# Kernel tuning notes

Measured on AMD Instinct MI355X. Metric: run time of the kernel, lower is better.

## Reference

```python
import jax, jax.numpy as jnp
import numpy as np


def setup_inputs() -> dict:
    key = jax.random.key(0)
    ks = jax.random.split(key, 6)
    B, F, E, H, U = 64, 4096, 256, 512, 512
    scale = 0.02
    return {
        "features": jax.random.normal(ks[0], (B, F, E), dtype=jnp.float32),
        "hidden": jax.random.normal(ks[1], (B, H), dtype=jnp.float32),
        "W1_w": jax.random.normal(ks[2], (E, U), dtype=jnp.float32) * scale,
        "W1_b": jnp.zeros((U,), dtype=jnp.float32),
        "W2_w": jax.random.normal(ks[3], (H, U), dtype=jnp.float32) * scale,
        "W2_b": jnp.zeros((U,), dtype=jnp.float32),
        "V_w": jax.random.normal(ks[4], (U, 1), dtype=jnp.float32) * scale,
        "V_b": jnp.zeros((1,), dtype=jnp.float32),
    }


def reference(features, hidden, W1_w, W1_b, W2_w, W2_b, V_w, V_b):
    # features: (B, F, E); hidden: (B, H)
    proj_f = jnp.einsum("bfe,eu->bfu", features, W1_w) + W1_b          # (B, F, U)
    proj_h = (hidden @ W2_w + W2_b)[:, None, :]                        # (B, 1, U)
    attention_hidden = jnp.tanh(proj_f + proj_h)                       # (B, F, U)
    scores = jnp.einsum("bfu,uo->bfo", attention_hidden, V_w) + V_b    # (B, F, 1)
    attention_weights = jax.nn.softmax(scores, axis=1)                 # (B, F, 1)
    context_vector = jnp.sum(attention_weights * features, axis=1)     # (B, E)
    return (context_vector, attention_weights)
```

## Files before the change

### kernel.cpp

```cpp
#include <hip/hip_runtime.h>
#include <cmath>

constexpr int Bdim = 64;
constexpr int Fdim = 4096;
constexpr int Edim = 256;
constexpr int Hdim = 512;
constexpr int Udim = 512;

typedef __attribute__((ext_vector_type(8))) short short8;
typedef __attribute__((ext_vector_type(4))) float f32x4;

__device__ __forceinline__ unsigned short f2bf(float f) {
    unsigned int u = __float_as_uint(f);
    u += 0x7FFFu + ((u >> 16) & 1u);
    return (unsigned short)(u >> 16);
}
__device__ __forceinline__ unsigned int pack2(float lo, float hi) {
    return (unsigned int)f2bf(lo) | ((unsigned int)f2bf(hi) << 16);
}
__device__ __forceinline__ float tanh_fast(float x) {
    float e = __expf(2.0f * x);
    return 1.0f - 2.0f * __builtin_amdgcn_rcpf(e + 1.0f);
}
__device__ __forceinline__ void gload_lds16(const void* g, void* l) {
    __builtin_amdgcn_global_load_lds(
        (const __attribute__((address_space(1))) unsigned int*)g,
        (__attribute__((address_space(3))) unsigned int*)l, 16, 0, 0);
}

__global__ __launch_bounds__(256) void prep_kernel(
    const float* __restrict__ hidden, const float* __restrict__ W2,
    const float* __restrict__ W1b, const float* __restrict__ W2b,
    float* __restrict__ cb,
    const float* __restrict__ W1, unsigned short* __restrict__ Th,
    float* __restrict__ ctx, const int do_t)
{
    const int bid = blockIdx.x;
    const int tid = threadIdx.x;

    if (bid < 128) {
        const int b = bid >> 1;
        const int u = (bid & 1) * 256 + tid;
        const float* hb = hidden + (size_t)b * Hdim;
        float acc = 0.f;
        #pragma unroll 8
        for (int h = 0; h < Hdim; ++h)
            acc = fmaf(hb[h], W2[(size_t)h * Udim + u], acc);
        cb[(size_t)b * Udim + u] = acc + W1b[u] + W2b[u];
    } else if (bid < 160) {
        if (!do_t) return;
        __shared__ unsigned short sT[64][72];
        const int k  = bid - 128;
        const int e0 = (k & 3) * 64, u0 = (k >> 2) * 64;
        const int ue = tid & 63, er = tid >> 6;
        #pragma unroll
        for (int it = 0; it < 16; ++it) {
            const int e = er + it * 4;
            sT[ue][e] = f2bf(W1[(size_t)(e0 + e) * Udim + u0 + ue]);
        }
        __syncthreads();
        const int ur = tid >> 2, cq = tid & 3;
        const int u = u0 + ur, s = u & 7;
        const int cA = (e0 >> 3) + cq * 2;
        uint4 a  = *(const uint4*)&sT[ur][cq * 16];
        uint4 b2 = *(const uint4*)&sT[ur][cq * 16 + 8];
        unsigned short* dst = Th + (size_t)u * Edim;
        *(uint4*)(dst + ((cA ^ s) << 3))       = a;
        *(uint4*)(dst + (((cA + 1) ^ s) << 3)) = b2;
    } else {
        const int idx = (bid - 160) * 256 + tid;
        ((float4*)ctx)[idx] = make_float4(0.f, 0.f, 0.f, 0.f);
    }
}

__global__ __launch_bounds__(256, 4) void score_mfma4_kernel(
    const float* __restrict__ feat,
    const unsigned short* __restrict__ W1Ts,
    const float* __restrict__ Vw, const float* __restrict__ Vb,
    const float* __restrict__ cb, float* __restrict__ scr)
{
    __shared__ unsigned short lds[16896];

    const int b    = blockIdx.y;
    const int f0   = blockIdx.x * 64;
    const int tid  = threadIdx.x;
    const int lane = tid & 63;
    const int w    = tid >> 6;
    const int ln15 = lane & 15;
    const int kq   = lane >> 4;
    const int swz  = ln15 & 7;

    short8 af[8];
    {
        unsigned short* sAw = lds + w * 4224;
        const float* gA = feat + ((size_t)(b * Fdim + f0 + w * 16)) * Edim;
        #pragma unroll
        for (int r = 0; r < 16; ++r) {
            float4 v = *(const float4*)(gA + (size_t)r * Edim + lane * 4);
            uint2 p; p.x = pack2(v.x, v.y); p.y = pack2(v.z, v.w);
            *(uint2*)&sAw[r * 264 + lane * 4] = p;
        }
        #pragma unroll
        for (int k8 = 0; k8 < 8; ++k8)
            af[k8] = *(const short8*)&sAw[ln15 * 264 + k8 * 32 + kq * 8];
    }
    __syncthreads();

    float sacc[4] = {};
    const float* cbB = cb + (size_t)b * Udim;

    {
        const char* gB = (const char*)W1Ts;
        #pragma unroll
        for (int t = 0; t < 4; ++t) {
            const int chunk = w * 4 + t;
            gload_lds16(gB + (size_t)chunk * 1024 + lane * 16,
                        (char*)lds + chunk * 1024);
        }
    }
    __syncthreads();

    for (int p = 0; p < 16; ++p) {
        if (p < 15) {
            const char* gB = (const char*)(W1Ts + (size_t)(p + 1) * 32 * Edim);
            char* lb = (char*)lds + ((p + 1) & 1) * 16384;
            #pragma unroll
            for (int t = 0; t < 4; ++t) {
                const int chunk = w * 4 + t;
                gload_lds16(gB + (size_t)chunk * 1024 + lane * 16,
                            lb + chunk * 1024);
            }
        }

        const unsigned short* bw = lds + (p & 1) * 8192;
        const int ub = p * 32;
        const float cu0 = cbB[ub + ln15],     cu1 = cbB[ub + 16 + ln15];
        const float vv0 = Vw[ub + ln15],      vv1 = Vw[ub + 16 + ln15];
        f32x4 acc0 = {}, acc1 = {};
        #pragma unroll
        for (int k8 = 0; k8 < 8; ++k8) {
            const int co = ((k8 * 4 + kq) ^ swz) * 8;
            short8 b0 = *(const short8*)&bw[ln15 * 256 + co];
            short8 b1 = *(const short8*)&bw[(16 + ln15) * 256 + co];
            acc0 = __builtin_amdgcn_mfma_f32_16x16x32_bf16(af[k8], b0, acc0, 0, 0, 0);
            acc1 = __builtin_amdgcn_mfma_f32_16x16x32_bf16(af[k8], b1, acc1, 0, 0, 0);
        }
        #pragma unroll
        for (int r = 0; r < 4; ++r)
            sacc[r] += tanh_fast(acc0[r] + cu0) * vv0
                     + tanh_fast(acc1[r] + cu1) * vv1;

        if (p < 15) __syncthreads();
    }

    const float vb = Vb[0];
    #pragma unroll
    for (int r = 0; r < 4; ++r) {
        float s = sacc[r];
        s += __shfl_xor(s, 1);
        s += __shfl_xor(s, 2);
        s += __shfl_xor(s, 4);
        s += __shfl_xor(s, 8);
        if (ln15 == 0)
            scr[(size_t)b * Fdim + f0 + w * 16 + kq * 4 + r] = s + vb;
    }
}

__global__ __launch_bounds__(256) void ctxnorm_kernel(
    const float* __restrict__ feat, const float* __restrict__ scr,
    float* __restrict__ wts, float* __restrict__ ctx)
{
    __shared__ float  red[8];
    __shared__ float  wl[256];
    __shared__ float4 sred[256];

    const int b   = blockIdx.y;
    const int fc  = blockIdx.x;
    const int f0  = fc * 256;
    const int tid = threadIdx.x;
    const float* row = scr + (size_t)b * Fdim;

    float v[16];
    float m = -INFINITY;
    #pragma unroll
    for (int i = 0; i < 16; ++i) {
        v[i] = row[tid + 256 * i];
        m = fmaxf(m, v[i]);
    }
    #pragma unroll
    for (int off = 1; off < 64; off <<= 1)
        m = fmaxf(m, __shfl_xor(m, off));
    if ((tid & 63) == 0) red[tid >> 6] = m;
    __syncthreads();
    m = fmaxf(fmaxf(red[0], red[1]), fmaxf(red[2], red[3]));

    float s = 0.f;
    #pragma unroll
    for (int i = 0; i < 16; ++i)
        s += expf(v[i] - m);
    #pragma unroll
    for (int off = 1; off < 64; off <<= 1)
        s += __shfl_xor(s, off);
    if ((tid & 63) == 0) red[4 + (tid >> 6)] = s;
    __syncthreads();
    const float inv = 1.0f / (red[4] + red[5] + red[6] + red[7]);

    const float wgt = expf(v[fc] - m) * inv;
    wts[(size_t)b * Fdim + f0 + tid] = wgt;
    wl[tid] = wgt;
    __syncthreads();

    const int e4 = tid & 63;
    const int fg = tid >> 6;
    const float4* fp = (const float4*)(feat + ((size_t)b * Fdim + f0) * Edim);

    float4 a = make_float4(0.f, 0.f, 0.f, 0.f);
    #pragma unroll 8
    for (int i = 0; i < 64; ++i) {
        const int f = i * 4 + fg;
        const float4 fv = fp[(size_t)f * 64 + e4];
        const float wv = wl[f];
        a.x = fmaf(wv, fv.x, a.x);
        a.y = fmaf(wv, fv.y, a.y);
        a.z = fmaf(wv, fv.z, a.z);
        a.w = fmaf(wv, fv.w, a.w);
    }
    sred[tid] = a;
    __syncthreads();

    if (fg == 0) {
        const float4 r0 = sred[e4];
        const float4 r1 = sred[64 + e4];
        const float4 r2 = sred[128 + e4];
        const float4 r3 = sred[192 + e4];
        float* cp = ctx + (size_t)b * Edim + e4 * 4;
        atomicAdd(cp + 0, r0.x + r1.x + r2.x + r3.x);
        atomicAdd(cp + 1, r0.y + r1.y + r2.y + r3.y);
        atomicAdd(cp + 2, r0.z + r1.z + r2.z + r3.z);
        atomicAdd(cp + 3, r0.w + r1.w + r2.w + r3.w);
    }
}

constexpr int TFt = 64;
constexpr int TUt = 64;
constexpr int LDR = Edim + 4;

__global__ __launch_bounds__(256) void score_kernel(
    const float* __restrict__ feat, const float* __restrict__ W1,
    const float* __restrict__ Vw, const float* __restrict__ Vb,
    const float* __restrict__ cb, float* __restrict__ scores)
{
    __shared__ float sA[TFt * LDR];
    __shared__ float sW[TUt * LDR];

    const int b   = blockIdx.y;
    const int f0  = blockIdx.x * TFt;
    const int tid = threadIdx.x;
    const int tf  = tid >> 4;
    const int tu  = tid & 15;

    {
        const float4* gA = (const float4*)(feat + ((size_t)b * Fdim + f0) * Edim);
        #pragma unroll
        for (int it = 0; it < 16; ++it) {
            const int i = tid + it * 256;
            const int f = i >> 6;
            const int qq = i & 63;
            const float4 v = gA[i];
            *(float4*)&sA[f * LDR + 4 * qq] = v;
        }
    }

    float sacc[4] = {0.f, 0.f, 0.f, 0.f};
    const float* cbb = cb + (size_t)b * Udim;

    for (int uc = 0; uc < Udim; uc += TUt) {
        __syncthreads();
        #pragma unroll
        for (int it = 0; it < 16; ++it) {
            const int i = tid + it * 256;
            const int e = i >> 4;
            const int qq = i & 15;
            const float4 v = *(const float4*)(W1 + (size_t)e * Udim + uc + 4 * qq);
            sW[(4 * qq + 0) * LDR + e] = v.x;
            sW[(4 * qq + 1) * LDR + e] = v.y;
            sW[(4 * qq + 2) * LDR + e] = v.z;
            sW[(4 * qq + 3) * LDR + e] = v.w;
        }
        __syncthreads();

        float acc[4][4] = {};
        #pragma unroll 4
        for (int e = 0; e < Edim; e += 4) {
            float4 a0 = *(const float4*)&sA[(tf +  0) * LDR + e];
            float4 a1 = *(const float4*)&sA[(tf + 16) * LDR + e];
            float4 a2 = *(const float4*)&sA[(tf + 32) * LDR + e];
            float4 a3 = *(const float4*)&sA[(tf + 48) * LDR + e];
            float4 w0 = *(const float4*)&sW[(tu +  0) * LDR + e];
            float4 w1 = *(const float4*)&sW[(tu + 16) * LDR + e];
            float4 w2 = *(const float4*)&sW[(tu + 32) * LDR + e];
            float4 w3 = *(const float4*)&sW[(tu + 48) * LDR + e];
            #define FMA4(i, j, A, W)                         \
                acc[i][j] = fmaf(A.x, W.x, acc[i][j]);       \
                acc[i][j] = fmaf(A.y, W.y, acc[i][j]);       \
                acc[i][j] = fmaf(A.z, W.z, acc[i][j]);       \
                acc[i][j] = fmaf(A.w, W.w, acc[i][j]);
            FMA4(0,0,a0,w0) FMA4(0,1,a0,w1) FMA4(0,2,a0,w2) FMA4(0,3,a0,w3)
            FMA4(1,0,a1,w0) FMA4(1,1,a1,w1) FMA4(1,2,a1,w2) FMA4(1,3,a1,w3)
            FMA4(2,0,a2,w0) FMA4(2,1,a2,w1) FMA4(2,2,a2,w2) FMA4(2,3,a2,w3)
            FMA4(3,0,a3,w0) FMA4(3,1,a3,w1) FMA4(3,2,a3,w2) FMA4(3,3,a3,w3)
            #undef FMA4
        }

        #pragma unroll
        for (int j = 0; j < 4; ++j) {
            const int u = uc + tu + 16 * j;
            const float vw = Vw[u];
            const float cuv = cbb[u];
            #pragma unroll
            for (int i = 0; i < 4; ++i)
                sacc[i] = fmaf(tanhf(acc[i][j] + cuv), vw, sacc[i]);
        }
    }

    const float vb = Vb[0];
    #pragma unroll
    for (int i = 0; i < 4; ++i) {
        float s = sacc[i];
        s += __shfl_xor(s, 1);
        s += __shfl_xor(s, 2);
        s += __shfl_xor(s, 4);
        s += __shfl_xor(s, 8);
        if (tu == 0)
            scores[(size_t)b * Fdim + f0 + tf + 16 * i] = s + vb;
    }
}

__global__ __launch_bounds__(256) void softmax_kernel(float* __restrict__ sc)
{
    __shared__ float red[256];
    const int b = blockIdx.x;
    const int tid = threadIdx.x;
    float* row = sc + (size_t)b * Fdim;

    float v[16];
    float m = -INFINITY;
    #pragma unroll
    for (int i = 0; i < 16; ++i) {
        v[i] = row[tid + 256 * i];
        m = fmaxf(m, v[i]);
    }
    red[tid] = m;
    __syncthreads();
    for (int s = 128; s > 0; s >>= 1) {
        if (tid < s) red[tid] = fmaxf(red[tid], red[tid + s]);
        __syncthreads();
    }
    m = red[0];
    __syncthreads();

    float sum = 0.f;
    #pragma unroll
    for (int i = 0; i < 16; ++i) {
        v[i] = expf(v[i] - m);
        sum += v[i];
    }
    red[tid] = sum;
    __syncthreads();
    for (int s = 128; s > 0; s >>= 1) {
        if (tid < s) red[tid] += red[tid + s];
        __syncthreads();
    }
    const float inv = 1.f / red[0];
    #pragma unroll
    for (int i = 0; i < 16; ++i)
        row[tid + 256 * i] = v[i] * inv;
}

__global__ __launch_bounds__(256) void context_kernel(
    const float* __restrict__ feat, const float* __restrict__ wts,
    float* __restrict__ ctx)
{
    const int b  = blockIdx.y;
    const int fc = blockIdx.x;
    const int e  = threadIdx.x;

    const float* fp = feat + ((size_t)b * Fdim + (size_t)fc * 256) * Edim + e;
    const float* wp = wts + (size_t)b * Fdim + (size_t)fc * 256;

    float acc = 0.f;
    #pragma unroll 8
    for (int f = 0; f < 256; ++f)
        acc = fmaf(wp[f], fp[(size_t)f * Edim], acc);

    atomicAdd(&ctx[(size_t)b * Edim + e], acc);
}

extern "C" void kernel_launch(void* const* d_in, const int* in_sizes, int n_in,
                              void* d_out, int out_size, void* d_ws, size_t ws_size,
                              hipStream_t stream)
{
    const float* features = (const float*)d_in[0];
    const float* hidden   = (const float*)d_in[1];
    const float* W1w      = (const float*)d_in[2];
    const float* W1b      = (const float*)d_in[3];
    const float* W2w      = (const float*)d_in[4];
    const float* W2b      = (const float*)d_in[5];
    const float* Vw       = (const float*)d_in[6];
    const float* Vb       = (const float*)d_in[7];

    float* ctx = (float*)d_out;
    float* wts = (float*)d_out + (size_t)Bdim * Edim;

    float*          cb   = (float*)d_ws;
    unsigned short* W1Ts = (unsigned short*)((char*)d_ws + 131072);
    float*          scr  = (float*)((char*)d_ws + 131072 + 262144);
    const size_t NEED = 131072 + 262144 + (size_t)Bdim * Fdim * sizeof(float);
    const int mfma_ok = (ws_size >= NEED) ? 1 : 0;

    prep_kernel<<<176, 256, 0, stream>>>(hidden, W2w, W1b, W2b, cb,
                                         W1w, W1Ts, ctx, mfma_ok);

    if (mfma_ok) {
        dim3 sgrid(Fdim / 64, Bdim);
        score_mfma4_kernel<<<sgrid, 256, 0, stream>>>(features, W1Ts, Vw, Vb, cb, scr);
        dim3 cgrid(Fdim / 256, Bdim);
        ctxnorm_kernel<<<cgrid, 256, 0, stream>>>(features, scr, wts, ctx);
    } else {
        dim3 sgrid(Fdim / TFt, Bdim);
        score_kernel<<<sgrid, 256, 0, stream>>>(features, W1w, Vw, Vb, cb, wts);
        softmax_kernel<<<Bdim, 256, 0, stream>>>(wts);
        dim3 cgrid(16, Bdim);
        context_kernel<<<cgrid, 256, 0, stream>>>(features, wts, ctx);
    }
}
```

Baseline: 481.3 us.

## Fuse context accumulation into score kernel via online-softmax partials and merge

Folds the context-vector pass into the MFMA score kernel. Each 64-feature tile computes a local max, a local exp-sum and an unnormalised weighted feature sum, and a small per-batch merge kernel rescales and combines these partials and writes the final weights. This avoids re-reading the full 256 MB feature tensor in a second kernel, since the tile is still hot in cache, and removes the float atomics. The cost is extra workspace for the partials, some added epilogue work in the score kernel, and extra LDS reuse with barriers.

Measured after the change: 464.6 us. 1.04x faster.

```diff
diff --git a/kernel.cpp b/kernel.cpp
--- a/kernel.cpp
+++ b/kernel.cpp
@@ -77,12 +77,14 @@
     const float* __restrict__ feat,
     const unsigned short* __restrict__ W1Ts,
     const float* __restrict__ Vw, const float* __restrict__ Vb,
-    const float* __restrict__ cb, float* __restrict__ scr)
+    const float* __restrict__ cb, float* __restrict__ scr,
+    float* __restrict__ pm, float* __restrict__ ps, float* __restrict__ pc)
 {
     __shared__ unsigned short lds[16896];
 
     const int b    = blockIdx.y;
-    const int f0   = blockIdx.x * 64;
+    const int fc   = blockIdx.x;
+    const int f0   = fc * 64;
     const int tid  = threadIdx.x;
     const int lane = tid & 63;
     const int w    = tid >> 6;
@@ -153,6 +155,10 @@
         if (p < 15) __syncthreads();
     }
 
+    float* sF = (float*)lds;
+    float* wl = (float*)lds + 64;
+    float4* sred = (float4*)((char*)lds + 1024);
+
     const float vb = Vb[0];
     #pragma unroll
     for (int r = 0; r < 4; ++r) {
@@ -161,53 +167,32 @@
         s += __shfl_xor(s, 2);
         s += __shfl_xor(s, 4);
         s += __shfl_xor(s, 8);
-        if (ln15 == 0)
-            scr[(size_t)b * Fdim + f0 + w * 16 + kq * 4 + r] = s + vb;
-    }
-}
-
-__global__ __launch_bounds__(256) void ctxnorm_kernel(
-    const float* __restrict__ feat, const float* __restrict__ scr,
-    float* __restrict__ wts, float* __restrict__ ctx)
-{
-    __shared__ float  red[8];
-    __shared__ float  wl[256];
-    __shared__ float4 sred[256];
-
-    const int b   = blockIdx.y;
-    const int fc  = blockIdx.x;
-    const int f0  = fc * 256;
-    const int tid = threadIdx.x;
-    const float* row = scr + (size_t)b * Fdim;
-
-    float v[16];
-    float m = -INFINITY;
-    #pragma unroll
-    for (int i = 0; i < 16; ++i) {
-        v[i] = row[tid + 256 * i];
-        m = fmaxf(m, v[i]);
-    }
-    #pragma unroll
-    for (int off = 1; off < 64; off <<= 1)
-        m = fmaxf(m, __shfl_xor(m, off));
-    if ((tid & 63) == 0) red[tid >> 6] = m;
-    __syncthreads();
-    m = fmaxf(fmaxf(red[0], red[1]), fmaxf(red[2], red[3]));
-
-    float s = 0.f;
-    #pragma unroll
-    for (int i = 0; i < 16; ++i)
-        s += expf(v[i] - m);
-    #pragma unroll
-    for (int off = 1; off < 64; off <<= 1)
-        s += __shfl_xor(s, off);
-    if ((tid & 63) == 0) red[4 + (tid >> 6)] = s;
-    __syncthreads();
-    const float inv = 1.0f / (red[4] + red[5] + red[6] + red[7]);
-
-    const float wgt = expf(v[fc] - m) * inv;
-    wts[(size_t)b * Fdim + f0 + tid] = wgt;
-    wl[tid] = wgt;
+        if (ln15 == 0) {
+            const int fr = w * 16 + kq * 4 + r;
+            const float sv = s + vb;
+            scr[(size_t)b * Fdim + f0 + fr] = sv;
+            sF[fr] = sv;
+        }
+    }
+    __syncthreads();
+
+    if (tid < 64) {
+        const float sc = sF[tid];
+        float m = sc;
+        #pragma unroll
+        for (int off = 1; off < 64; off <<= 1)
+            m = fmaxf(m, __shfl_xor(m, off));
+        const float wv = expf(sc - m);
+        float sm = wv;
+        #pragma unroll
+        for (int off = 1; off < 64; off <<= 1)
+            sm += __shfl_xor(sm, off);
+        wl[tid] = wv;
+        if (tid == 0) {
+            pm[b * 64 + fc] = m;
+            ps[b * 64 + fc] = sm;
+        }
+    }
     __syncthreads();
 
     const int e4 = tid & 63;
@@ -215,8 +200,8 @@
     const float4* fp = (const float4*)(feat + ((size_t)b * Fdim + f0) * Edim);
 
     float4 a = make_float4(0.f, 0.f, 0.f, 0.f);
-    #pragma unroll 8
-    for (int i = 0; i < 64; ++i) {
+    #pragma unroll
+    for (int i = 0; i < 16; ++i) {
         const int f = i * 4 + fg;
         const float4 fv = fp[(size_t)f * 64 + e4];
         const float wv = wl[f];
@@ -233,11 +218,59 @@
         const float4 r1 = sred[64 + e4];
         const float4 r2 = sred[128 + e4];
         const float4 r3 = sred[192 + e4];
-        float* cp = ctx + (size_t)b * Edim + e4 * 4;
-        atomicAdd(cp + 0, r0.x + r1.x + r2.x + r3.x);
-        atomicAdd(cp + 1, r0.y + r1.y + r2.y + r3.y);
-        atomicAdd(cp + 2, r0.z + r1.z + r2.z + r3.z);
-        atomicAdd(cp + 3, r0.w + r1.w + r2.w + r3.w);
+        float4 o;
+        o.x = r0.x + r1.x + r2.x + r3.x;
+        o.y = r0.y + r1.y + r2.y + r3.y;
+        o.z = r0.z + r1.z + r2.z + r3.z;
+        o.w = r0.w + r1.w + r2.w + r3.w;
+        *(float4*)&pc[((size_t)b * 64 + fc) * 256 + e4 * 4] = o;
+    }
+}
+
+__global__ __launch_bounds__(256) void merge_kernel(
+    const float* __restrict__ scr, const float* __restrict__ pm,
+    const float* __restrict__ ps, const float* __restrict__ pc,
+    float* __restrict__ wts, float* __restrict__ ctx)
+{
+    __shared__ float sscale[64];
+    __shared__ float sms[2];
+
+    const int b   = blockIdx.x;
+    const int tid = threadIdx.x;
+
+    if (tid < 64) {
+        const float mi = pm[b * 64 + tid];
+        float m = mi;
+        #pragma unroll
+        for (int off = 1; off < 64; off <<= 1)
+            m = fmaxf(m, __shfl_xor(m, off));
+        const float sc = expf(mi - m);
+        float s = ps[b * 64 + tid] * sc;
+        #pragma unroll
+        for (int off = 1; off < 64; off <<= 1)
+            s += __shfl_xor(s, off);
+        sscale[tid] = sc;
+        if (tid == 0) { sms[0] = m; sms[1] = 1.0f / s; }
+    }
+    __syncthreads();
+    const float m   = sms[0];
+    const float inv = sms[1];
+
+    {
+        float c = 0.f;
+        const float* p = pc + (size_t)b * 64 * 256 + tid;
+        #pragma unroll 8
+        for (int i = 0; i < 64; ++i)
+            c = fmaf(p[(size_t)i * 256], sscale[i], c);
+        ctx[(size_t)b * Edim + tid] = c * inv;
+    }
+
+    const float* row  = scr + (size_t)b * Fdim;
+    float*       wrow = wts + (size_t)b * Fdim;
+    #pragma unroll
+    for (int i = 0; i < 16; ++i) {
+        const float v = row[tid + 256 * i];
+        wrow[tid + 256 * i] = expf(v - m) * inv;
     }
 }
 
@@ -414,8 +447,11 @@
 
     float*          cb   = (float*)d_ws;
     unsigned short* W1Ts = (unsigned short*)((char*)d_ws + 131072);
-    float*          scr  = (float*)((char*)d_ws + 131072 + 262144);
-    const size_t NEED = 131072 + 262144 + (size_t)Bdim * Fdim * sizeof(float);
+    float*          scr  = (float*)((char*)d_ws + 393216);
+    float*          pm   = (float*)((char*)d_ws + 1441792);
+    float*          ps   = (float*)((char*)d_ws + 1458176);
+    float*          pc   = (float*)((char*)d_ws + 1474560);
+    const size_t NEED = 1474560 + (size_t)Bdim * 64 * Edim * sizeof(float);
     const int mfma_ok = (ws_size >= NEED) ? 1 : 0;
 
     prep_kernel<<<176, 256, 0, stream>>>(hidden, W2w, W1b, W2b, cb,
@@ -423,9 +459,9 @@
 
     if (mfma_ok) {
         dim3 sgrid(Fdim / 64, Bdim);
-        score_mfma4_kernel<<<sgrid, 256, 0, stream>>>(features, W1Ts, Vw, Vb, cb, scr);
-        dim3 cgrid(Fdim / 256, Bdim);
-        ctxnorm_kernel<<<cgrid, 256, 0, stream>>>(features, scr, wts, ctx);
+        score_mfma4_kernel<<<sgrid, 256, 0, stream>>>(features, W1Ts, Vw, Vb, cb,
+                                                      scr, pm, ps, pc);
+        merge_kernel<<<Bdim, 256, 0, stream>>>(scr, pm, ps, pc, wts, ctx);
     } else {
         dim3 sgrid(Fdim / TFt, Bdim);
         score_kernel<<<sgrid, 256, 0, stream>>>(features, W1w, Vw, Vb, cb, wts);
```
